# Optimization experiments

Hardware: AMD Instinct MI355X
Metric: run time of the kernel (lower is better)

## Reference

```python
import jax, jax.numpy as jnp
import numpy as np

N_HEAD = 8
N_GROUPS = 4
EPS = 1e-5


def setup_inputs() -> dict:
    key = jax.random.key(0)
    ks = jax.random.split(key, 4)
    B, C, D, H, W = 4, 256, 32, 32, 32
    x = jax.random.normal(ks[0], (B, C, D, H, W), dtype=jnp.float32)
    gamma = jnp.ones((C,), dtype=jnp.float32)
    beta = jnp.zeros((C,), dtype=jnp.float32)
    # 1x1 Conv3d == channel matmul; fan-in scaled init
    w_qkv = jax.random.normal(ks[1], (3 * C, C), dtype=jnp.float32) / np.sqrt(C)
    w_out = jax.random.normal(ks[2], (C, C), dtype=jnp.float32) / np.sqrt(C)
    b_out = jnp.zeros((C,), dtype=jnp.float32)
    return {"x": x, "gamma": gamma, "beta": beta, "w_qkv": w_qkv,
            "w_out": w_out, "b_out": b_out}


def _group_norm(x, gamma, beta):
    B, C = x.shape[0], x.shape[1]
    xg = x.reshape(B, N_GROUPS, C // N_GROUPS, *x.shape[2:])
    mu = xg.mean(axis=(2, 3, 4, 5), keepdims=True)
    var = xg.var(axis=(2, 3, 4, 5), keepdims=True)
    xn = ((xg - mu) * jax.lax.rsqrt(var + EPS)).reshape(x.shape)
    return xn * gamma[None, :, None, None, None] + beta[None, :, None, None, None]


def reference(x, gamma, beta, w_qkv, w_out, b_out):
    B, C, D, H, W = x.shape
    n = D * H * W
    dh = C // N_HEAD
    norm = _group_norm(x, gamma, beta)                       # [B,C,D,H,W]
    flat = norm.reshape(B, C, n)                             # [B,C,n]
    qkv = jnp.einsum('oc,bcn->bon', w_qkv, flat)             # [B,3C,n]
    q, k, v = jnp.split(qkv, 3, axis=1)
    q = q.reshape(B, N_HEAD, dh, n)
    k = k.reshape(B, N_HEAD, dh, n)
    v = v.reshape(B, N_HEAD, dh, n)
    k = jax.nn.softmax(k, axis=-1)                           # over tokens n
    q = jax.nn.softmax(q, axis=-2)                           # over head dim d
    context = jnp.einsum('bhdn,bhen->bhde', k, v)            # [B,h,d,d]
    out = jnp.einsum('bhde,bhdn->bhen', context, q)          # [B,h,d,n]
    out = out.reshape(B, C, n)
    out = jnp.einsum('oc,bcn->bon', w_out, out) + b_out[None, :, None]
    return out.reshape(B, C, D, H, W) + x
```

## Files before the change

kernel.cpp:

```cpp
#include <hip/hip_runtime.h>
#include <hip/hip_bf16.h>
#include <math.h>

#define NTOK  32768
#define GNEPS 1e-5f

typedef __attribute__((ext_vector_type(4))) float f32x4;
typedef __attribute__((ext_vector_type(8))) short s16x8;
typedef __attribute__((ext_vector_type(4))) unsigned short u16x4;

__device__ __forceinline__ unsigned short f2b(float f) {
  unsigned int u = __float_as_uint(f);
  unsigned int r = (u + 0x7FFFu + ((u >> 16) & 1u)) >> 16;
  return (unsigned short)r;
}
__device__ __forceinline__ float b2f(unsigned short s) {
  return __uint_as_float(((unsigned int)s) << 16);
}

__device__ __forceinline__ void stage16(const unsigned short* g, unsigned short* ldsChunkBase, int lane) {
#if __has_builtin(__builtin_amdgcn_global_load_lds)
  __builtin_amdgcn_global_load_lds((const __attribute__((address_space(1))) void*)g,
                                   (__attribute__((address_space(3))) void*)ldsChunkBase, 16, 0, 0);
#else
  *(s16x8*)((char*)ldsChunkBase + lane * 16) = *(const s16x8*)g;
#endif
}

#define OFF_GSTAT   0u
#define OFF_SSUM    4224u
#define OFF_CTX     8320u
#define OFF_WCTXB   139392u
#define OFF_BIASP   663680u
#define OFF_WP      675968u
#define OFF_XT      2248832u
#define OFF_QT      69357696u
#define OFF_KVB     136466560u
#define WS_NEEDED   (OFF_KVB + 134217728ull)

__global__ __launch_bounds__(256) void gn_fused(const float* __restrict__ x,
                                                float* __restrict__ gstat,
                                                unsigned short* __restrict__ xT) {
  __shared__ unsigned short s1[256 * 64];
  __shared__ float rs[4][4], rq[4][4];
  int b = blockIdx.y;
  int n0 = blockIdx.x * 64;
  int tid = threadIdx.x;
  const float* xb = x + (size_t)b * 256 * NTOK;
  float s[4] = {0.f, 0.f, 0.f, 0.f}, sq[4] = {0.f, 0.f, 0.f, 0.f};
#pragma unroll
  for (int it = 0; it < 16; ++it) {
    int idx = tid + it * 256;
    int c = idx >> 4, q = idx & 15;
    f32x4 v = *reinterpret_cast<const f32x4*>(&xb[(size_t)c * NTOK + n0 + q * 4]);
    const int g = it >> 2;
    s[g]  += v.x + v.y + v.z + v.w;
    sq[g] += v.x * v.x + v.y * v.y + v.z * v.z + v.w * v.w;
    u16x4 o = { f2b(v.x), f2b(v.y), f2b(v.z), f2b(v.w) };
    int phys = (q * 4 + (c >> 3) * 4) & 63;
    *reinterpret_cast<u16x4*>(&s1[c * 64 + phys]) = o;
  }
  int lane = tid & 63, w = tid >> 6;
#pragma unroll
  for (int g = 0; g < 4; ++g) {
    float a = s[g], bq = sq[g];
    for (int o = 32; o > 0; o >>= 1) { a += __shfl_down(a, o); bq += __shfl_down(bq, o); }
    if (lane == 0) { rs[w][g] = a; rq[w][g] = bq; }
  }
  __syncthreads();
  if (tid < 8) {
    int g = tid >> 1, part = tid & 1;
    float v = part ? (rq[0][g] + rq[1][g] + rq[2][g] + rq[3][g])
                   : (rs[0][g] + rs[1][g] + rs[2][g] + rs[3][g]);
    atomicAdd(&gstat[2 * (b * 4 + g) + part], v);
  }
#pragma unroll
  for (int it = 0; it < 8; ++it) {
    int task = tid + it * 256;
    int n = task >> 5, oc = task & 31;
    int phys = (n + oc * 4) & 63;
    s16x8 pk;
#pragma unroll
    for (int i = 0; i < 8; ++i) pk[i] = (short)s1[(oc * 8 + i) * 64 + phys];
    *reinterpret_cast<s16x8*>(&xT[((size_t)(b * NTOK + n0 + n)) * 256 + oc * 8]) = pk;
  }
}

__global__ __launch_bounds__(256) void fold_w(const float* __restrict__ wqkv,
                                              const float* __restrict__ gamma,
                                              const float* __restrict__ beta,
                                              const float* __restrict__ gstat,
                                              unsigned short* __restrict__ Wp,
                                              float* __restrict__ biasp) {
  int o = blockIdx.x, b = blockIdx.y;
  int c = threadIdx.x;
  int g = c >> 6;
  const float cnt = 64.f * (float)NTOK;
  float mu  = gstat[2 * (b * 4 + g)] / cnt;
  float var = gstat[2 * (b * 4 + g) + 1] / cnt - mu * mu;
  float rsig = rsqrtf(var + GNEPS);
  float wv = wqkv[(size_t)o * 256 + c];
  float A = gamma[c] * rsig;
  float Bc = beta[c] - mu * A;
  Wp[((size_t)b * 768 + o) * 256 + c] = f2b(wv * A);
  float t = wv * Bc;
  int lane = c & 63, w = c >> 6;
  for (int off = 32; off > 0; off >>= 1) t += __shfl_down(t, off);
  __shared__ float red[4];
  if (lane == 0) red[w] = t;
  __syncthreads();
  if (c == 0) biasp[b * 768 + o] = red[0] + red[1] + red[2] + red[3];
}

__global__ __launch_bounds__(512, 4) void qkv_gemm(const unsigned short* __restrict__ Wp,
                                                   const float* __restrict__ biasp,
                                                   const unsigned short* __restrict__ xT,
                                                   unsigned short* __restrict__ qT,
                                                   unsigned short* __restrict__ kvb) {
  __shared__ unsigned short smem[24576];
  unsigned short* As = smem;
  unsigned short* Bs = smem + 16384;
  int bid = blockIdx.x;
  int L = (bid & 7) * 384 + (bid >> 3);
  int ot = L % 3;
  int t2 = L / 3;
  int b = t2 & 3, nt = t2 >> 2;
  int n0 = nt * 128;
  int tid = threadIdx.x;
  int w = tid >> 6, l = tid & 63;
  int hi = (l >> 4) & 3, lo = l & 15;
  int wo = w >> 1, wn = w & 1;
  int lr = l >> 3, lj = l & 7;
  int srcj = lj ^ lr;
  const unsigned short* Abase = Wp + ((size_t)(b * 768 + ot * 256)) * 256;
  const unsigned short* Bbase = xT + ((size_t)(b * NTOK + n0)) * 256;

  f32x4 acc[4][4];
#pragma unroll
  for (int s = 0; s < 4; ++s)
#pragma unroll
    for (int n = 0; n < 4; ++n) acc[s][n] = (f32x4){0.f, 0.f, 0.f, 0.f};

  for (int c0 = 0; c0 < 256; c0 += 64) {
    __syncthreads();
#pragma unroll
    for (int q = 0; q < 4; ++q) {
      int chunk = w * 4 + q; int row = chunk * 8 + lr;
      stage16(Abase + (size_t)row * 256 + c0 + srcj * 8, As + chunk * 512, l);
    }
#pragma unroll
    for (int q = 0; q < 2; ++q) {
      int chunk = w * 2 + q; int row = chunk * 8 + lr;
      stage16(Bbase + (size_t)row * 256 + c0 + srcj * 8, Bs + chunk * 512, l);
    }
    __syncthreads();
#pragma unroll
    for (int t = 0; t < 2; ++t) {
      s16x8 af[4], bf[4];
#pragma unroll
      for (int s = 0; s < 4; ++s) {
        int row = wo * 64 + s * 16 + lo;
        int phys = (t * 4 + hi) ^ (row & 7);
        af[s] = *reinterpret_cast<const s16x8*>(&As[row * 64 + phys * 8]);
      }
#pragma unroll
      for (int n = 0; n < 4; ++n) {
        int row = wn * 64 + n * 16 + lo;
        int phys = (t * 4 + hi) ^ (row & 7);
        bf[n] = *reinterpret_cast<const s16x8*>(&Bs[row * 64 + phys * 8]);
      }
#pragma unroll
      for (int s = 0; s < 4; ++s)
#pragma unroll
        for (int n = 0; n < 4; ++n)
          acc[s][n] = __builtin_amdgcn_mfma_f32_16x16x32_bf16(af[s], bf[n], acc[s][n], 0, 0, 0);
    }
  }

#pragma unroll
  for (int s = 0; s < 4; ++s)
#pragma unroll
    for (int i = 0; i < 4; ++i) {
      float bv = biasp[b * 768 + ot * 256 + wo * 64 + s * 16 + hi * 4 + i];
#pragma unroll
      for (int n = 0; n < 4; ++n) acc[s][n][i] += bv;
    }

  if (ot == 0) {
    for (int r = 0; r < 2; ++r) {
      __syncthreads();
      if (wn == r) {
#pragma unroll
        for (int s = 0; s < 4; ++s)
#pragma unroll
          for (int n = 0; n < 4; ++n)
#pragma unroll
            for (int i = 0; i < 4; ++i) {
              int o_l = wo * 64 + s * 16 + hi * 4 + i;
              int n_l = n * 16 + lo;
              smem[n_l * 264 + o_l] = f2b(acc[s][n][i]);
            }
      }
      __syncthreads();
      {
        int n_l = tid >> 3, h = tid & 7;
        unsigned short* rowp = &smem[n_l * 264 + h * 32];
        float v[32];
        float m = -1e30f;
#pragma unroll
        for (int i = 0; i < 32; ++i) { v[i] = b2f(rowp[i]); m = fmaxf(m, v[i]); }
        float ssum = 0.f;
#pragma unroll
        for (int i = 0; i < 32; ++i) { v[i] = __expf(v[i] - m); ssum += v[i]; }
        float rr = 1.f / ssum;
#pragma unroll
        for (int i = 0; i < 32; ++i) rowp[i] = f2b(v[i] * rr);
      }
      __syncthreads();
#pragma unroll
      for (int it = 0; it < 4; ++it) {
        int task = tid + it * 512;
        int n_l = task >> 5, j = task & 31;
        s16x8 v = *reinterpret_cast<const s16x8*>(&smem[n_l * 264 + j * 8]);
        *reinterpret_cast<s16x8*>(&qT[((size_t)(b * NTOK + n0 + r * 64 + n_l)) * 256 + j * 8]) = v;
      }
    }
  } else {
    int vbase = (ot == 1) ? 0 : 256;
    for (int r = 0; r < 2; ++r) {
      __syncthreads();
      if ((wo >> 1) == r) {
#pragma unroll
        for (int s = 0; s < 4; ++s)
#pragma unroll
          for (int n = 0; n < 4; ++n)
#pragma unroll
            for (int i = 0; i < 4; ++i) {
              int o_l = (wo & 1) * 64 + s * 16 + hi * 4 + i;
              int n_l = wn * 64 + n * 16 + lo;
              smem[o_l * 136 + n_l] = f2b(acc[s][n][i]);
            }
      }
      __syncthreads();
#pragma unroll
      for (int it = 0; it < 4; ++it) {
        int task = tid + it * 512;
        int o_l = task >> 4, j = task & 15;
        s16x8 v = *reinterpret_cast<const s16x8*>(&smem[o_l * 136 + j * 8]);
        int row = vbase + r * 128 + o_l;
        *reinterpret_cast<s16x8*>(&kvb[((size_t)(b * 512 + row)) * NTOK + n0 + j * 8]) = v;
      }
    }
  }
}

__global__ __launch_bounds__(256) void context_mfma(const unsigned short* __restrict__ kvb,
                                                    float* __restrict__ ctx,
                                                    float* __restrict__ Ssum) {
  __shared__ unsigned short kl[32 * 512];
  __shared__ unsigned short vl[32 * 512];
  int bh = blockIdx.y;
  int b = bh >> 3, h = bh & 7;
  int n0 = blockIdx.x * 512;
  int tid = threadIdx.x;
  int w = tid >> 6, l = tid & 63;
  int lo = l & 15, hi = l >> 4;
  const unsigned short* kb = kvb + (((size_t)(b * 512) + h * 32) * NTOK) + n0;
  const unsigned short* vb = kvb + (((size_t)(b * 512) + 256 + h * 32) * NTOK) + n0;

#pragma unroll
  for (int it = 0; it < 8; ++it) {
    int task = tid + it * 256;
    int row = task >> 6, blk = task & 63;
    int phys = blk ^ (row & 7);
    s16x8 kv = *reinterpret_cast<const s16x8*>(&kb[(size_t)row * NTOK + blk * 8]);
    s16x8 vv = *reinterpret_cast<const s16x8*>(&vb[(size_t)row * NTOK + blk * 8]);
    s16x8 ke;
#pragma unroll
    for (int j = 0; j < 8; ++j) ke[j] = (short)f2b(__expf(b2f((unsigned short)kv[j])));
    *reinterpret_cast<s16x8*>(&kl[row * 512 + phys * 8]) = ke;
    *reinterpret_cast<s16x8*>(&vl[row * 512 + phys * 8]) = vv;
  }
  __syncthreads();

  f32x4 acc[2][2], accS[2];
#pragma unroll
  for (int fr = 0; fr < 2; ++fr) {
    accS[fr] = (f32x4){0.f, 0.f, 0.f, 0.f};
#pragma unroll
    for (int fc = 0; fc < 2; ++fc) acc[fr][fc] = (f32x4){0.f, 0.f, 0.f, 0.f};
  }
  s16x8 ones;
#pragma unroll
  for (int j = 0; j < 8; ++j) ones[j] = (short)0x3F80;

#pragma unroll
  for (int ks = 0; ks < 4; ++ks) {
    int nblk = w * 16 + ks * 4 + hi;
    s16x8 af[2], bf[2];
#pragma unroll
    for (int fr = 0; fr < 2; ++fr) {
      int row = fr * 16 + lo;
      int phys = nblk ^ (row & 7);
      af[fr] = *reinterpret_cast<const s16x8*>(&kl[row * 512 + phys * 8]);
      bf[fr] = *reinterpret_cast<const s16x8*>(&vl[row * 512 + phys * 8]);
    }
#pragma unroll
    for (int fr = 0; fr < 2; ++fr) {
#pragma unroll
      for (int fc = 0; fc < 2; ++fc)
        acc[fr][fc] = __builtin_amdgcn_mfma_f32_16x16x32_bf16(af[fr], bf[fc], acc[fr][fc], 0, 0, 0);
      accS[fr] = __builtin_amdgcn_mfma_f32_16x16x32_bf16(af[fr], ones, accS[fr], 0, 0, 0);
    }
  }
  __syncthreads();

  float* lpart = reinterpret_cast<float*>(kl);
  float* mine = lpart + w * 1056;
#pragma unroll
  for (int fr = 0; fr < 2; ++fr) {
#pragma unroll
    for (int fc = 0; fc < 2; ++fc)
#pragma unroll
      for (int i = 0; i < 4; ++i) {
        int row = fr * 16 + hi * 4 + i;
        int col = fc * 16 + lo;
        mine[row * 32 + col] = acc[fr][fc][i];
      }
    if (lo == 0)
#pragma unroll
      for (int i = 0; i < 4; ++i)
        mine[1024 + fr * 16 + hi * 4 + i] = accS[fr][i];
  }
  __syncthreads();
  float* cb = ctx + (size_t)bh * 1024;
  for (int i = tid; i < 1024; i += 256) {
    float v = lpart[i] + lpart[1056 + i] + lpart[2112 + i] + lpart[3168 + i];
    atomicAdd(&cb[i], v);
  }
  if (tid < 32) {
    int i = 1024 + tid;
    float v = lpart[i] + lpart[1056 + i] + lpart[2112 + i] + lpart[3168 + i];
    atomicAdd(&Ssum[b * 256 + h * 32 + tid], v);
  }
}

__global__ __launch_bounds__(256) void make_wctx(const float* __restrict__ wout,
                                                 const float* __restrict__ ctx,
                                                 const float* __restrict__ Ssum,
                                                 unsigned short* __restrict__ wctxb) {
  int o = blockIdx.x, b = blockIdx.y;
  int tid = threadIdx.x;
  int h = tid >> 5, d = tid & 31;
  const float* cb = ctx + ((size_t)(b * 8 + h)) * 1024 + d * 32;
  const float* wr = wout + (size_t)o * 256 + h * 32;
  float s = 0.f;
#pragma unroll
  for (int e = 0; e < 32; ++e) s += wr[e] * cb[e];
  s *= (1.f / Ssum[b * 256 + tid]);
  wctxb[((size_t)b * 256 + o) * 256 + tid] = f2b(s);
}

__global__ __launch_bounds__(512, 4) void out_gemm(const unsigned short* __restrict__ wctxb,
                                                   const unsigned short* __restrict__ qT,
                                                   const float* __restrict__ bout,
                                                   const float* __restrict__ x,
                                                   float* __restrict__ out) {
  __shared__ unsigned short smem[24576];
  unsigned short* As = smem;
  unsigned short* Bs = smem + 16384;
  int bid = blockIdx.x;
  int L = (bid & 7) * 128 + (bid >> 3);
  int b = L >> 8, nt = L & 255;
  int n0 = nt * 128;
  int tid = threadIdx.x;
  int w = tid >> 6, l = tid & 63;
  int hi = (l >> 4) & 3, lo = l & 15;
  int wo = w >> 1, wn = w & 1;
  int lr = l >> 3, lj = l & 7;
  int srcj = lj ^ lr;
  const unsigned short* Abase = wctxb + (size_t)b * 65536;
  const unsigned short* Bbase = qT + ((size_t)(b * NTOK + n0)) * 256;

  f32x4 acc[4][4];
#pragma unroll
  for (int s = 0; s < 4; ++s)
#pragma unroll
    for (int n = 0; n < 4; ++n) acc[s][n] = (f32x4){0.f, 0.f, 0.f, 0.f};

  for (int c0 = 0; c0 < 256; c0 += 64) {
    __syncthreads();
#pragma unroll
    for (int q = 0; q < 4; ++q) {
      int chunk = w * 4 + q; int row = chunk * 8 + lr;
      stage16(Abase + (size_t)row * 256 + c0 + srcj * 8, As + chunk * 512, l);
    }
#pragma unroll
    for (int q = 0; q < 2; ++q) {
      int chunk = w * 2 + q; int row = chunk * 8 + lr;
      stage16(Bbase + (size_t)row * 256 + c0 + srcj * 8, Bs + chunk * 512, l);
    }
    __syncthreads();
#pragma unroll
    for (int t = 0; t < 2; ++t) {
      s16x8 af[4], bf[4];
#pragma unroll
      for (int s = 0; s < 4; ++s) {
        int row = wo * 64 + s * 16 + lo;
        int phys = (t * 4 + hi) ^ (row & 7);
        af[s] = *reinterpret_cast<const s16x8*>(&As[row * 64 + phys * 8]);
      }
#pragma unroll
      for (int n = 0; n < 4; ++n) {
        int row = wn * 64 + n * 16 + lo;
        int phys = (t * 4 + hi) ^ (row & 7);
        bf[n] = *reinterpret_cast<const s16x8*>(&Bs[row * 64 + phys * 8]);
      }
#pragma unroll
      for (int s = 0; s < 4; ++s)
#pragma unroll
        for (int n = 0; n < 4; ++n)
          acc[s][n] = __builtin_amdgcn_mfma_f32_16x16x32_bf16(af[s], bf[n], acc[s][n], 0, 0, 0);
    }
  }

  float* bounce = reinterpret_cast<float*>(smem);
  const float* xb = x + (size_t)b * 256 * NTOK;
  for (int r = 0; r < 4; ++r) {
    __syncthreads();
    if (wo == r) {
#pragma unroll
      for (int s = 0; s < 4; ++s)
#pragma unroll
        for (int n = 0; n < 4; ++n)
#pragma unroll
          for (int i = 0; i < 4; ++i) {
            int o_l = s * 16 + hi * 4 + i;
            int n_l = wn * 64 + n * 16 + lo;
            bounce[o_l * 132 + n_l] = acc[s][n][i];
          }
    }
    __syncthreads();
#pragma unroll
    for (int it = 0; it < 4; ++it) {
      int task = tid + it * 512;
      int o_l = task >> 5, q4 = task & 31;
      int o = r * 64 + o_l;
      f32x4 a = *reinterpret_cast<const f32x4*>(&bounce[o_l * 132 + q4 * 4]);
      f32x4 xv = *reinterpret_cast<const f32x4*>(&xb[(size_t)o * NTOK + n0 + q4 * 4]);
      float bo = bout[o];
      f32x4 rlt = { a.x + bo + xv.x, a.y + bo + xv.y, a.z + bo + xv.z, a.w + bo + xv.w };
      *reinterpret_cast<f32x4*>(&out[((size_t)b * 256 + o) * NTOK + n0 + q4 * 4]) = rlt;
    }
  }
}

extern "C" void kernel_launch(void* const* d_in, const int* in_sizes, int n_in,
                              void* d_out, int out_size, void* d_ws, size_t ws_size,
                              hipStream_t stream) {
  const float* x     = (const float*)d_in[0];
  const float* gamma = (const float*)d_in[1];
  const float* beta  = (const float*)d_in[2];
  const float* wqkv  = (const float*)d_in[3];
  const float* wout  = (const float*)d_in[4];
  const float* bout  = (const float*)d_in[5];
  float* out = (float*)d_out;

  if (ws_size < WS_NEEDED) return;

  char* ws = (char*)d_ws;
  float* gstat        = (float*)(ws + OFF_GSTAT);
  float* Ssum         = (float*)(ws + OFF_SSUM);
  float* ctx          = (float*)(ws + OFF_CTX);
  unsigned short* wctxb = (unsigned short*)(ws + OFF_WCTXB);
  float* biasp        = (float*)(ws + OFF_BIASP);
  unsigned short* Wp  = (unsigned short*)(ws + OFF_WP);
  unsigned short* xT  = (unsigned short*)(ws + OFF_XT);
  unsigned short* qT  = (unsigned short*)(ws + OFF_QT);
  unsigned short* kvb = (unsigned short*)(ws + OFF_KVB);

  hipMemsetAsync(ws, 0, OFF_CTX + 131072u, stream);

  gn_fused  <<<dim3(512, 4), 256, 0, stream>>>(x, gstat, xT);
  fold_w    <<<dim3(768, 4), 256, 0, stream>>>(wqkv, gamma, beta, gstat, Wp, biasp);
  qkv_gemm  <<<3072, 512, 0, stream>>>(Wp, biasp, xT, qT, kvb);
  context_mfma<<<dim3(64, 32), 256, 0, stream>>>(kvb, ctx, Ssum);
  make_wctx <<<dim3(256, 4), 256, 0, stream>>>(wout, ctx, Ssum, wctxb);
  out_gemm  <<<1024, 512, 0, stream>>>(wctxb, qT, bout, x, out);
}
```

Measured before the change: 253.6 us.

## Fuse K/V projection with context accumulation to skip the KV round trip

Splits the QKV GEMM into a Q-only GEMM and a new kv_ctx kernel. The new kernel computes K and V tiles in LDS, applies exp to K, and accumulates the context and softmax denominators directly with MFMA. This removes the 128 MB bf16 K/V buffer write and its read-back by a separate context kernel. The cost is a fused kernel with smaller 64-token tiles, 72 KB of dynamic LDS, more syncthreads, and more per-lane global atomics in place of the earlier LDS pre-reduction.

```diff
diff --git a/kernel.cpp b/kernel.cpp
--- a/kernel.cpp
+++ b/kernel.cpp
@@ -35,8 +35,7 @@
 #define OFF_WP      675968u
 #define OFF_XT      2248832u
 #define OFF_QT      69357696u
-#define OFF_KVB     136466560u
-#define WS_NEEDED   (OFF_KVB + 134217728ull)
+#define WS_NEEDED   (OFF_QT + 67108864ull)
 
 __global__ __launch_bounds__(256) void gn_fused(const float* __restrict__ x,
                                                 float* __restrict__ gstat,
@@ -112,19 +111,16 @@
   if (c == 0) biasp[b * 768 + o] = red[0] + red[1] + red[2] + red[3];
 }
 
-__global__ __launch_bounds__(512, 4) void qkv_gemm(const unsigned short* __restrict__ Wp,
-                                                   const float* __restrict__ biasp,
-                                                   const unsigned short* __restrict__ xT,
-                                                   unsigned short* __restrict__ qT,
-                                                   unsigned short* __restrict__ kvb) {
+__global__ __launch_bounds__(512, 4) void q_gemm(const unsigned short* __restrict__ Wp,
+                                                 const float* __restrict__ biasp,
+                                                 const unsigned short* __restrict__ xT,
+                                                 unsigned short* __restrict__ qT) {
   __shared__ unsigned short smem[24576];
   unsigned short* As = smem;
   unsigned short* Bs = smem + 16384;
   int bid = blockIdx.x;
-  int L = (bid & 7) * 384 + (bid >> 3);
-  int ot = L % 3;
-  int t2 = L / 3;
-  int b = t2 & 3, nt = t2 >> 2;
+  int L = (bid & 7) * 128 + (bid >> 3);
+  int b = L >> 8, nt = L & 255;
   int n0 = nt * 128;
   int tid = threadIdx.x;
   int w = tid >> 6, l = tid & 63;
@@ -132,7 +128,7 @@
   int wo = w >> 1, wn = w & 1;
   int lr = l >> 3, lj = l & 7;
   int srcj = lj ^ lr;
-  const unsigned short* Abase = Wp + ((size_t)(b * 768 + ot * 256)) * 256;
+  const unsigned short* Abase = Wp + ((size_t)(b * 768)) * 256;
   const unsigned short* Bbase = xT + ((size_t)(b * NTOK + n0)) * 256;
 
   f32x4 acc[4][4];
@@ -181,167 +177,186 @@
   for (int s = 0; s < 4; ++s)
 #pragma unroll
     for (int i = 0; i < 4; ++i) {
-      float bv = biasp[b * 768 + ot * 256 + wo * 64 + s * 16 + hi * 4 + i];
+      float bv = biasp[b * 768 + wo * 64 + s * 16 + hi * 4 + i];
 #pragma unroll
       for (int n = 0; n < 4; ++n) acc[s][n][i] += bv;
     }
 
-  if (ot == 0) {
-    for (int r = 0; r < 2; ++r) {
-      __syncthreads();
-      if (wn == r) {
-#pragma unroll
-        for (int s = 0; s < 4; ++s)
-#pragma unroll
-          for (int n = 0; n < 4; ++n)
-#pragma unroll
-            for (int i = 0; i < 4; ++i) {
-              int o_l = wo * 64 + s * 16 + hi * 4 + i;
-              int n_l = n * 16 + lo;
-              smem[n_l * 264 + o_l] = f2b(acc[s][n][i]);
-            }
-      }
-      __syncthreads();
-      {
-        int n_l = tid >> 3, h = tid & 7;
-        unsigned short* rowp = &smem[n_l * 264 + h * 32];
-        float v[32];
-        float m = -1e30f;
-#pragma unroll
-        for (int i = 0; i < 32; ++i) { v[i] = b2f(rowp[i]); m = fmaxf(m, v[i]); }
-        float ssum = 0.f;
-#pragma unroll
-        for (int i = 0; i < 32; ++i) { v[i] = __expf(v[i] - m); ssum += v[i]; }
-        float rr = 1.f / ssum;
-#pragma unroll
-        for (int i = 0; i < 32; ++i) rowp[i] = f2b(v[i] * rr);
-      }
-      __syncthreads();
-#pragma unroll
-      for (int it = 0; it < 4; ++it) {
-        int task = tid + it * 512;
-        int n_l = task >> 5, j = task & 31;
-        s16x8 v = *reinterpret_cast<const s16x8*>(&smem[n_l * 264 + j * 8]);
-        *reinterpret_cast<s16x8*>(&qT[((size_t)(b * NTOK + n0 + r * 64 + n_l)) * 256 + j * 8]) = v;
-      }
-    }
-  } else {
-    int vbase = (ot == 1) ? 0 : 256;
-    for (int r = 0; r < 2; ++r) {
-      __syncthreads();
-      if ((wo >> 1) == r) {
-#pragma unroll
-        for (int s = 0; s < 4; ++s)
-#pragma unroll
-          for (int n = 0; n < 4; ++n)
-#pragma unroll
-            for (int i = 0; i < 4; ++i) {
-              int o_l = (wo & 1) * 64 + s * 16 + hi * 4 + i;
-              int n_l = wn * 64 + n * 16 + lo;
-              smem[o_l * 136 + n_l] = f2b(acc[s][n][i]);
-            }
-      }
-      __syncthreads();
-#pragma unroll
-      for (int it = 0; it < 4; ++it) {
-        int task = tid + it * 512;
-        int o_l = task >> 4, j = task & 15;
-        s16x8 v = *reinterpret_cast<const s16x8*>(&smem[o_l * 136 + j * 8]);
-        int row = vbase + r * 128 + o_l;
-        *reinterpret_cast<s16x8*>(&kvb[((size_t)(b * 512 + row)) * NTOK + n0 + j * 8]) = v;
-      }
-    }
-  }
-}
-
-__global__ __launch_bounds__(256) void context_mfma(const unsigned short* __restrict__ kvb,
-                                                    float* __restrict__ ctx,
-                                                    float* __restrict__ Ssum) {
-  __shared__ unsigned short kl[32 * 512];
-  __shared__ unsigned short vl[32 * 512];
-  int bh = blockIdx.y;
-  int b = bh >> 3, h = bh & 7;
-  int n0 = blockIdx.x * 512;
+  for (int r = 0; r < 2; ++r) {
+    __syncthreads();
+    if (wn == r) {
+#pragma unroll
+      for (int s = 0; s < 4; ++s)
+#pragma unroll
+        for (int n = 0; n < 4; ++n)
+#pragma unroll
+          for (int i = 0; i < 4; ++i) {
+            int o_l = wo * 64 + s * 16 + hi * 4 + i;
+            int n_l = n * 16 + lo;
+            smem[n_l * 264 + o_l] = f2b(acc[s][n][i]);
+          }
+    }
+    __syncthreads();
+    {
+      int n_l = tid >> 3, h = tid & 7;
+      unsigned short* rowp = &smem[n_l * 264 + h * 32];
+      float v[32];
+      float m = -1e30f;
+#pragma unroll
+      for (int i = 0; i < 32; ++i) { v[i] = b2f(rowp[i]); m = fmaxf(m, v[i]); }
+      float ssum = 0.f;
+#pragma unroll
+      for (int i = 0; i < 32; ++i) { v[i] = __expf(v[i] - m); ssum += v[i]; }
+      float rr = 1.f / ssum;
+#pragma unroll
+      for (int i = 0; i < 32; ++i) rowp[i] = f2b(v[i] * rr);
+    }
+    __syncthreads();
+#pragma unroll
+    for (int it = 0; it < 4; ++it) {
+      int task = tid + it * 512;
+      int n_l = task >> 5, j = task & 31;
+      s16x8 v = *reinterpret_cast<const s16x8*>(&smem[n_l * 264 + j * 8]);
+      *reinterpret_cast<s16x8*>(&qT[((size_t)(b * NTOK + n0 + r * 64 + n_l)) * 256 + j * 8]) = v;
+    }
+  }
+}
+
+__global__ __launch_bounds__(512, 4) void kv_ctx(const unsigned short* __restrict__ Wp,
+                                                 const float* __restrict__ biasp,
+                                                 const unsigned short* __restrict__ xT,
+                                                 float* __restrict__ ctx,
+                                                 float* __restrict__ Ssum) {
+  extern __shared__ unsigned short dyn[];
+  unsigned short* E  = dyn;
+  unsigned short* As = dyn + 16384;
+  unsigned short* Bs = dyn + 32768;
+  unsigned short* V  = As;
+  int bid = blockIdx.x;
+  int L = (bid & 7) * 64 + (bid >> 3);
+  int b = L >> 7;
+  int ntbase = (L & 127) * 4;
   int tid = threadIdx.x;
   int w = tid >> 6, l = tid & 63;
-  int lo = l & 15, hi = l >> 4;
-  const unsigned short* kb = kvb + (((size_t)(b * 512) + h * 32) * NTOK) + n0;
-  const unsigned short* vb = kvb + (((size_t)(b * 512) + 256 + h * 32) * NTOK) + n0;
-
-#pragma unroll
-  for (int it = 0; it < 8; ++it) {
-    int task = tid + it * 256;
-    int row = task >> 6, blk = task & 63;
-    int phys = blk ^ (row & 7);
-    s16x8 kv = *reinterpret_cast<const s16x8*>(&kb[(size_t)row * NTOK + blk * 8]);
-    s16x8 vv = *reinterpret_cast<const s16x8*>(&vb[(size_t)row * NTOK + blk * 8]);
-    s16x8 ke;
-#pragma unroll
-    for (int j = 0; j < 8; ++j) ke[j] = (short)f2b(__expf(b2f((unsigned short)kv[j])));
-    *reinterpret_cast<s16x8*>(&kl[row * 512 + phys * 8]) = ke;
-    *reinterpret_cast<s16x8*>(&vl[row * 512 + phys * 8]) = vv;
-  }
-  __syncthreads();
-
-  f32x4 acc[2][2], accS[2];
+  int hi = (l >> 4) & 3, lo = l & 15;
+  int wo = w >> 1, wn = w & 1;
+  int lr = l >> 3, lj = l & 7;
+  int srcj = lj ^ lr;
+  int h = w;
+
+  f32x4 acc_ctx[2][2], accS[2];
 #pragma unroll
   for (int fr = 0; fr < 2; ++fr) {
     accS[fr] = (f32x4){0.f, 0.f, 0.f, 0.f};
 #pragma unroll
-    for (int fc = 0; fc < 2; ++fc) acc[fr][fc] = (f32x4){0.f, 0.f, 0.f, 0.f};
+    for (int fc = 0; fc < 2; ++fc) acc_ctx[fr][fc] = (f32x4){0.f, 0.f, 0.f, 0.f};
   }
   s16x8 ones;
 #pragma unroll
   for (int j = 0; j < 8; ++j) ones[j] = (short)0x3F80;
 
-#pragma unroll
-  for (int ks = 0; ks < 4; ++ks) {
-    int nblk = w * 16 + ks * 4 + hi;
-    s16x8 af[2], bf[2];
-#pragma unroll
-    for (int fr = 0; fr < 2; ++fr) {
-      int row = fr * 16 + lo;
-      int phys = nblk ^ (row & 7);
-      af[fr] = *reinterpret_cast<const s16x8*>(&kl[row * 512 + phys * 8]);
-      bf[fr] = *reinterpret_cast<const s16x8*>(&vl[row * 512 + phys * 8]);
-    }
-#pragma unroll
-    for (int fr = 0; fr < 2; ++fr) {
-#pragma unroll
-      for (int fc = 0; fc < 2; ++fc)
-        acc[fr][fc] = __builtin_amdgcn_mfma_f32_16x16x32_bf16(af[fr], bf[fc], acc[fr][fc], 0, 0, 0);
-      accS[fr] = __builtin_amdgcn_mfma_f32_16x16x32_bf16(af[fr], ones, accS[fr], 0, 0, 0);
-    }
-  }
-  __syncthreads();
-
-  float* lpart = reinterpret_cast<float*>(kl);
-  float* mine = lpart + w * 1056;
+  for (int kt = 0; kt < 4; ++kt) {
+    int n0 = (ntbase + kt) * 64;
+    const unsigned short* Bbase = xT + ((size_t)(b * NTOK + n0)) * 256;
+
+#pragma unroll
+    for (int pass = 0; pass < 2; ++pass) {
+      const unsigned short* Abase = Wp + ((size_t)(b * 768 + 256 + pass * 256)) * 256;
+      f32x4 acc[4][2];
+#pragma unroll
+      for (int s = 0; s < 4; ++s)
+#pragma unroll
+        for (int n = 0; n < 2; ++n) acc[s][n] = (f32x4){0.f, 0.f, 0.f, 0.f};
+
+      for (int c0 = 0; c0 < 256; c0 += 64) {
+        __syncthreads();
+#pragma unroll
+        for (int q = 0; q < 4; ++q) {
+          int chunk = w * 4 + q; int row = chunk * 8 + lr;
+          stage16(Abase + (size_t)row * 256 + c0 + srcj * 8, As + chunk * 512, l);
+        }
+        {
+          int row = w * 8 + lr;
+          stage16(Bbase + (size_t)row * 256 + c0 + srcj * 8, Bs + w * 512, l);
+        }
+        __syncthreads();
+#pragma unroll
+        for (int t = 0; t < 2; ++t) {
+          s16x8 af[4], bf[2];
+#pragma unroll
+          for (int s = 0; s < 4; ++s) {
+            int row = wo * 64 + s * 16 + lo;
+            int phys = (t * 4 + hi) ^ (row & 7);
+            af[s] = *reinterpret_cast<const s16x8*>(&As[row * 64 + phys * 8]);
+          }
+#pragma unroll
+          for (int n = 0; n < 2; ++n) {
+            int row = wn * 32 + n * 16 + lo;
+            int phys = (t * 4 + hi) ^ (row & 7);
+            bf[n] = *reinterpret_cast<const s16x8*>(&Bs[row * 64 + phys * 8]);
+          }
+#pragma unroll
+          for (int s = 0; s < 4; ++s)
+#pragma unroll
+            for (int n = 0; n < 2; ++n)
+              acc[s][n] = __builtin_amdgcn_mfma_f32_16x16x32_bf16(af[s], bf[n], acc[s][n], 0, 0, 0);
+        }
+      }
+      if (pass == 1) __syncthreads();
+      unsigned short* dst = (pass == 0) ? E : V;
+#pragma unroll
+      for (int s = 0; s < 4; ++s)
+#pragma unroll
+        for (int i = 0; i < 4; ++i) {
+          int r = wo * 64 + s * 16 + hi * 4 + i;
+          float bv = biasp[b * 768 + 256 + pass * 256 + r];
+#pragma unroll
+          for (int n = 0; n < 2; ++n) {
+            int col = wn * 32 + n * 16 + lo;
+            float val = acc[s][n][i] + bv;
+            unsigned short ov = (pass == 0) ? f2b(__expf(val)) : f2b(val);
+            dst[r * 64 + (((col >> 3) ^ (r & 7)) << 3) + (col & 7)] = ov;
+          }
+        }
+    }
+    __syncthreads();
+
+#pragma unroll
+    for (int ks = 0; ks < 2; ++ks) {
+      s16x8 af[2], bf[2];
+#pragma unroll
+      for (int fr = 0; fr < 2; ++fr) {
+        int row = h * 32 + fr * 16 + lo;
+        int phys = (ks * 4 + hi) ^ (row & 7);
+        af[fr] = *reinterpret_cast<const s16x8*>(&E[row * 64 + phys * 8]);
+        bf[fr] = *reinterpret_cast<const s16x8*>(&V[row * 64 + phys * 8]);
+      }
+#pragma unroll
+      for (int fr = 0; fr < 2; ++fr) {
+#pragma unroll
+        for (int fc = 0; fc < 2; ++fc)
+          acc_ctx[fr][fc] = __builtin_amdgcn_mfma_f32_16x16x32_bf16(af[fr], bf[fc], acc_ctx[fr][fc], 0, 0, 0);
+        accS[fr] = __builtin_amdgcn_mfma_f32_16x16x32_bf16(af[fr], ones, accS[fr], 0, 0, 0);
+      }
+    }
+    __syncthreads();
+  }
+
+  float* cb = ctx + ((size_t)(b * 8 + h)) * 1024;
 #pragma unroll
   for (int fr = 0; fr < 2; ++fr) {
 #pragma unroll
     for (int fc = 0; fc < 2; ++fc)
 #pragma unroll
       for (int i = 0; i < 4; ++i) {
-        int row = fr * 16 + hi * 4 + i;
-        int col = fc * 16 + lo;
-        mine[row * 32 + col] = acc[fr][fc][i];
+        int d = fr * 16 + (l >> 4) * 4 + i;
+        int e = fc * 16 + lo;
+        atomicAdd(&cb[d * 32 + e], acc_ctx[fr][fc][i]);
       }
     if (lo == 0)
 #pragma unroll
       for (int i = 0; i < 4; ++i)
-        mine[1024 + fr * 16 + hi * 4 + i] = accS[fr][i];
-  }
-  __syncthreads();
-  float* cb = ctx + (size_t)bh * 1024;
-  for (int i = tid; i < 1024; i += 256) {
-    float v = lpart[i] + lpart[1056 + i] + lpart[2112 + i] + lpart[3168 + i];
-    atomicAdd(&cb[i], v);
-  }
-  if (tid < 32) {
-    int i = 1024 + tid;
-    float v = lpart[i] + lpart[1056 + i] + lpart[2112 + i] + lpart[3168 + i];
-    atomicAdd(&Ssum[b * 256 + h * 32 + tid], v);
+        atomicAdd(&Ssum[b * 256 + h * 32 + fr * 16 + (l >> 4) * 4 + i], accS[fr][i]);
   }
 }
 
@@ -477,14 +492,13 @@
   unsigned short* Wp  = (unsigned short*)(ws + OFF_WP);
   unsigned short* xT  = (unsigned short*)(ws + OFF_XT);
   unsigned short* qT  = (unsigned short*)(ws + OFF_QT);
-  unsigned short* kvb = (unsigned short*)(ws + OFF_KVB);
 
   hipMemsetAsync(ws, 0, OFF_CTX + 131072u, stream);
 
   gn_fused  <<<dim3(512, 4), 256, 0, stream>>>(x, gstat, xT);
   fold_w    <<<dim3(768, 4), 256, 0, stream>>>(wqkv, gamma, beta, gstat, Wp, biasp);
-  qkv_gemm  <<<3072, 512, 0, stream>>>(Wp, biasp, xT, qT, kvb);
-  context_mfma<<<dim3(64, 32), 256, 0, stream>>>(kvb, ctx, Ssum);
+  q_gemm    <<<1024, 512, 0, stream>>>(Wp, biasp, xT, qT);
+  kv_ctx    <<<512, 512, 73728, stream>>>(Wp, biasp, xT, ctx, Ssum);
   make_wctx <<<dim3(256, 4), 256, 0, stream>>>(wout, ctx, Ssum, wctxb);
   out_gemm  <<<1024, 512, 0, stream>>>(wctxb, qT, bout, x, out);
 }
```

New measurement: 332.9 us. 1.31x slower.

## Store K/V intermediates as fp8 and use fp8 MFMA for context

Applied to the files above, without the earlier changes.

The QKV GEMM epilogue now applies exp to K (scaled by 1/16) and writes K and V as fp8 in a pre-swizzled layout, halving the kvb intermediate buffer. The context kernel loads the tiles straight into LDS via global_load_lds and uses fp8 MFMA instructions, including an fp8 ones vector for row sums. This removes half the global traffic for K/V and moves the exp out of the context kernel. In exchange it loses precision (fp8 e4m3 for exp(k) and v), which risks accuracy, and the exp of unnormalised K may saturate fp8 even with the scale.

```diff
diff --git a/kernel.cpp b/kernel.cpp
--- a/kernel.cpp
+++ b/kernel.cpp
@@ -16,6 +16,25 @@
 }
 __device__ __forceinline__ float b2f(unsigned short s) {
   return __uint_as_float(((unsigned int)s) << 16);
+}
+__device__ __forceinline__ unsigned char f2f8(float f) {
+#if __has_builtin(__builtin_amdgcn_cvt_pk_fp8_f32)
+  return (unsigned char)(__builtin_amdgcn_cvt_pk_fp8_f32(f, f, 0, false) & 0xff);
+#else
+  unsigned int u = __float_as_uint(f);
+  unsigned int sgn = (u >> 24) & 0x80;
+  float af = fabsf(f);
+  if (af > 448.f) return (unsigned char)(sgn | 0x7E);
+  if (af < 1e-10f) return (unsigned char)sgn;
+  int e; float m = frexpf(af, &e);
+  int ee = e + 6;
+  if (ee < 1) { m = ldexpf(m, ee - 1); ee = 0; m *= 2.f; }
+  int mant = (int)(m * 16.f + 0.5f) - 8;
+  if (mant >= 8) { mant = 0; ee += 1; }
+  if (mant < 0) mant = 0;
+  if (ee > 15) return (unsigned char)(sgn | 0x7E);
+  return (unsigned char)(sgn | (ee << 3) | mant);
+#endif
 }
 
 __device__ __forceinline__ void stage16(const unsigned short* g, unsigned short* ldsChunkBase, int lane) {
@@ -24,6 +43,14 @@
                                    (__attribute__((address_space(3))) void*)ldsChunkBase, 16, 0, 0);
 #else
   *(s16x8*)((char*)ldsChunkBase + lane * 16) = *(const s16x8*)g;
+#endif
+}
+__device__ __forceinline__ void stage16b(const unsigned char* g, unsigned char* ldsChunkBase, int lane) {
+#if __has_builtin(__builtin_amdgcn_global_load_lds)
+  __builtin_amdgcn_global_load_lds((const __attribute__((address_space(1))) void*)g,
+                                   (__attribute__((address_space(3))) void*)ldsChunkBase, 16, 0, 0);
+#else
+  *(f32x4*)(ldsChunkBase + lane * 16) = *(const f32x4*)g;
 #endif
 }
 
@@ -36,7 +63,7 @@
 #define OFF_XT      2248832u
 #define OFF_QT      69357696u
 #define OFF_KVB     136466560u
-#define WS_NEEDED   (OFF_KVB + 134217728ull)
+#define WS_NEEDED   (OFF_KVB + 67108864ull)
 
 __global__ __launch_bounds__(256) void gn_fused(const float* __restrict__ x,
                                                 float* __restrict__ gstat,
@@ -116,7 +143,7 @@
                                                    const float* __restrict__ biasp,
                                                    const unsigned short* __restrict__ xT,
                                                    unsigned short* __restrict__ qT,
-                                                   unsigned short* __restrict__ kvb) {
+                                                   unsigned char* __restrict__ kvb8) {
   __shared__ unsigned short smem[24576];
   unsigned short* As = smem;
   unsigned short* Bs = smem + 16384;
@@ -226,6 +253,7 @@
       }
     }
   } else {
+    unsigned char* smem8 = reinterpret_cast<unsigned char*>(smem);
     int vbase = (ot == 1) ? 0 : 256;
     for (int r = 0; r < 2; ++r) {
       __syncthreads();
@@ -238,48 +266,49 @@
             for (int i = 0; i < 4; ++i) {
               int o_l = (wo & 1) * 64 + s * 16 + hi * 4 + i;
               int n_l = wn * 64 + n * 16 + lo;
-              smem[o_l * 136 + n_l] = f2b(acc[s][n][i]);
+              float val = acc[s][n][i];
+              smem8[o_l * 144 + n_l] = (ot == 1) ? f2f8(__expf(val) * 0.0625f)
+                                                 : f2f8(val);
             }
       }
       __syncthreads();
 #pragma unroll
-      for (int it = 0; it < 4; ++it) {
+      for (int it = 0; it < 2; ++it) {
         int task = tid + it * 512;
-        int o_l = task >> 4, j = task & 15;
-        s16x8 v = *reinterpret_cast<const s16x8*>(&smem[o_l * 136 + j * 8]);
+        int o_l = task >> 3, j = task & 7;
+        f32x4 v = *reinterpret_cast<const f32x4*>(&smem8[o_l * 144 + j * 16]);
         int row = vbase + r * 128 + o_l;
-        *reinterpret_cast<s16x8*>(&kvb[((size_t)(b * 512 + row)) * NTOK + n0 + j * 8]) = v;
-      }
-    }
-  }
-}
-
-__global__ __launch_bounds__(256) void context_mfma(const unsigned short* __restrict__ kvb,
+        int local16 = ((n0 & 511) >> 4) + j;
+        int phys16 = local16 ^ (row & 7);
+        *reinterpret_cast<f32x4*>(&kvb8[((size_t)(b * 512 + row)) * 32768
+                                        + (n0 & ~511) + phys16 * 16]) = v;
+      }
+    }
+  }
+}
+
+__global__ __launch_bounds__(256) void context_mfma(const unsigned char* __restrict__ kvb8,
                                                     float* __restrict__ ctx,
                                                     float* __restrict__ Ssum) {
-  __shared__ unsigned short kl[32 * 512];
-  __shared__ unsigned short vl[32 * 512];
+  __shared__ unsigned char ctile[32768];
+  unsigned char* kl = ctile;
+  unsigned char* vl = ctile + 16384;
   int bh = blockIdx.y;
   int b = bh >> 3, h = bh & 7;
   int n0 = blockIdx.x * 512;
   int tid = threadIdx.x;
   int w = tid >> 6, l = tid & 63;
   int lo = l & 15, hi = l >> 4;
-  const unsigned short* kb = kvb + (((size_t)(b * 512) + h * 32) * NTOK) + n0;
-  const unsigned short* vb = kvb + (((size_t)(b * 512) + 256 + h * 32) * NTOK) + n0;
-
-#pragma unroll
-  for (int it = 0; it < 8; ++it) {
-    int task = tid + it * 256;
-    int row = task >> 6, blk = task & 63;
-    int phys = blk ^ (row & 7);
-    s16x8 kv = *reinterpret_cast<const s16x8*>(&kb[(size_t)row * NTOK + blk * 8]);
-    s16x8 vv = *reinterpret_cast<const s16x8*>(&vb[(size_t)row * NTOK + blk * 8]);
-    s16x8 ke;
-#pragma unroll
-    for (int j = 0; j < 8; ++j) ke[j] = (short)f2b(__expf(b2f((unsigned short)kv[j])));
-    *reinterpret_cast<s16x8*>(&kl[row * 512 + phys * 8]) = ke;
-    *reinterpret_cast<s16x8*>(&vl[row * 512 + phys * 8]) = vv;
+  const unsigned char* kb = kvb8 + ((size_t)(b * 512 + h * 32)) * 32768 + n0;
+  const unsigned char* vb = kvb8 + ((size_t)(b * 512 + 256 + h * 32)) * 32768 + n0;
+
+#pragma unroll
+  for (int q = 0; q < 4; ++q) {
+    int chunk = w * 4 + q;
+    int row = chunk * 2 + (l >> 5);
+    int blk = l & 31;
+    stage16b(kb + (size_t)row * 32768 + blk * 16, kl + chunk * 1024, l);
+    stage16b(vb + (size_t)row * 32768 + blk * 16, vl + chunk * 1024, l);
   }
   __syncthreads();
 
@@ -290,32 +319,30 @@
 #pragma unroll
     for (int fc = 0; fc < 2; ++fc) acc[fr][fc] = (f32x4){0.f, 0.f, 0.f, 0.f};
   }
-  s16x8 ones;
-#pragma unroll
-  for (int j = 0; j < 8; ++j) ones[j] = (short)0x3F80;
+  long ones = 0x3838383838383838L;
 
 #pragma unroll
   for (int ks = 0; ks < 4; ++ks) {
-    int nblk = w * 16 + ks * 4 + hi;
-    s16x8 af[2], bf[2];
+    int tb = w * 16 + ks * 4 + hi;
+    long af[2], bf[2];
 #pragma unroll
     for (int fr = 0; fr < 2; ++fr) {
       int row = fr * 16 + lo;
-      int phys = nblk ^ (row & 7);
-      af[fr] = *reinterpret_cast<const s16x8*>(&kl[row * 512 + phys * 8]);
-      bf[fr] = *reinterpret_cast<const s16x8*>(&vl[row * 512 + phys * 8]);
+      int off = row * 512 + (((tb >> 1) ^ (row & 7)) << 4) + ((tb & 1) << 3);
+      af[fr] = *reinterpret_cast<const long*>(&kl[off]);
+      bf[fr] = *reinterpret_cast<const long*>(&vl[off]);
     }
 #pragma unroll
     for (int fr = 0; fr < 2; ++fr) {
 #pragma unroll
       for (int fc = 0; fc < 2; ++fc)
-        acc[fr][fc] = __builtin_amdgcn_mfma_f32_16x16x32_bf16(af[fr], bf[fc], acc[fr][fc], 0, 0, 0);
-      accS[fr] = __builtin_amdgcn_mfma_f32_16x16x32_bf16(af[fr], ones, accS[fr], 0, 0, 0);
+        acc[fr][fc] = __builtin_amdgcn_mfma_f32_16x16x32_fp8_fp8(af[fr], bf[fc], acc[fr][fc], 0, 0, 0);
+      accS[fr] = __builtin_amdgcn_mfma_f32_16x16x32_fp8_fp8(af[fr], ones, accS[fr], 0, 0, 0);
     }
   }
   __syncthreads();
 
-  float* lpart = reinterpret_cast<float*>(kl);
+  float* lpart = reinterpret_cast<float*>(ctile);
   float* mine = lpart + w * 1056;
 #pragma unroll
   for (int fr = 0; fr < 2; ++fr) {
@@ -477,14 +504,14 @@
   unsigned short* Wp  = (unsigned short*)(ws + OFF_WP);
   unsigned short* xT  = (unsigned short*)(ws + OFF_XT);
   unsigned short* qT  = (unsigned short*)(ws + OFF_QT);
-  unsigned short* kvb = (unsigned short*)(ws + OFF_KVB);
+  unsigned char* kvb8 = (unsigned char*)(ws + OFF_KVB);
 
   hipMemsetAsync(ws, 0, OFF_CTX + 131072u, stream);
 
   gn_fused  <<<dim3(512, 4), 256, 0, stream>>>(x, gstat, xT);
   fold_w    <<<dim3(768, 4), 256, 0, stream>>>(wqkv, gamma, beta, gstat, Wp, biasp);
-  qkv_gemm  <<<3072, 512, 0, stream>>>(Wp, biasp, xT, qT, kvb);
-  context_mfma<<<dim3(64, 32), 256, 0, stream>>>(kvb, ctx, Ssum);
+  qkv_gemm  <<<3072, 512, 0, stream>>>(Wp, biasp, xT, qT, kvb8);
+  context_mfma<<<dim3(64, 32), 256, 0, stream>>>(kvb8, ctx, Ssum);
   make_wctx <<<dim3(256, 4), 256, 0, stream>>>(wout, ctx, Ssum, wctxb);
   out_gemm  <<<1024, 512, 0, stream>>>(wctxb, qT, bout, x, out);
 }
```

After: 233.0 us. -8.1%, faster.
